# Performance work log

Measured on AMD Instinct MI355X. Metric: run time of the kernel, lower is better.

## Reference

```python
import jax, jax.numpy as jnp
import numpy as np
import math

EPS = float(np.finfo(np.float32).eps)
POWER = 4.0  # init power=4


def cube_face_uv(d):
    # OpenGL cube-map face selection: faces +x,-x,+y,-y,+z,-z -> 0..5
    x, y, z = d[:, 0], d[:, 1], d[:, 2]
    ax, ay, az = jnp.abs(x), jnp.abs(y), jnp.abs(z)
    is_x = (ax >= ay) & (ax >= az)
    is_y = (~is_x) & (ay >= az)
    ma = jnp.maximum(ax, jnp.maximum(ay, az))
    face = jnp.where(is_x, jnp.where(x > 0, 0, 1),
           jnp.where(is_y, jnp.where(y > 0, 2, 3), jnp.where(z > 0, 4, 5)))
    sc = jnp.where(is_x, jnp.where(x > 0, -z, z),
         jnp.where(is_y, x, jnp.where(z > 0, x, -x)))
    tc = jnp.where(is_x, -y, jnp.where(is_y, jnp.where(y > 0, z, -z), -y))
    s = 0.5 * (sc / ma + 1.0)
    t = 0.5 * (tc / ma + 1.0)
    return face.astype(jnp.int32), s, t


def bilinear(tex, face, s, t):
    # tex: [6,R,R,3]; clamp-to-edge bilinear at texel centers (i+0.5)/R
    R = tex.shape[1]
    u = s * R - 0.5
    v = t * R - 0.5
    u0 = jnp.floor(u); v0 = jnp.floor(v)
    fu = (u - u0)[:, None]; fv = (v - v0)[:, None]
    u0i = jnp.clip(u0.astype(jnp.int32), 0, R - 1)
    u1i = jnp.clip(u0.astype(jnp.int32) + 1, 0, R - 1)
    v0i = jnp.clip(v0.astype(jnp.int32), 0, R - 1)
    v1i = jnp.clip(v0.astype(jnp.int32) + 1, 0, R - 1)
    c00 = tex[face, v0i, u0i]; c01 = tex[face, v0i, u1i]
    c10 = tex[face, v1i, u0i]; c11 = tex[face, v1i, u1i]
    return (c00 * (1 - fu) + c01 * fu) * (1 - fv) + (c10 * (1 - fu) + c11 * fu) * fv


def setup_inputs() -> dict:
    key = jax.random.key(0)
    k1, k2, k3 = jax.random.split(key, 3)
    B, R = 1048576, 512
    viewdirs = jax.random.normal(k1, (B, 3), dtype=jnp.float32)
    viewdirs = viewdirs / (jnp.linalg.norm(viewdirs, axis=-1, keepdims=True) + 1e-8)
    saSample = jax.random.normal(k2, (B, 1), dtype=jnp.float32)
    # learned cubemap (init_val=-2 plus small noise so gradients are non-trivial)
    bg_mat = -2.0 + 0.1 * jax.random.normal(k3, (6, R, R, 3), dtype=jnp.float32)
    return {
        'viewdirs': viewdirs,
        'saSample': saSample,
        'bg_mat': bg_mat,
        'brightness': jnp.float32(0.0),
        'mul': jnp.float32(1.0),
        'mipbias': jnp.float32(0.5),
    }


def reference(viewdirs, saSample, bg_mat, brightness, mul, mipbias):
    R = bg_mat.shape[1]
    n_mips = int(math.log2(R)) + 1  # 10 for R=512
    # box-filter mip pyramid (as nvdiffrast auto-generates)
    pyr = [bg_mat]
    for _ in range(n_mips - 1):
        tex = pyr[-1]; r = tex.shape[1]
        pyr.append(tex.reshape(6, r // 2, 2, r // 2, 2, 3).mean(axis=(2, 4)))
    # sa2mip (mipnoise = 0)
    ainf = jnp.max(jnp.abs(viewdirs), axis=-1)            # ||u||_inf
    distortion = (1.0 / ainf)[:, None]                    # [B,1]
    saTexel = distortion / R / R
    mip = (saSample - jnp.log(jnp.clip(saTexel, EPS))) / math.log(POWER) / 2 + mipbias
    mip = jnp.clip(mip[:, 0], 0.0, n_mips - 1.0)          # [B]
    face, s, t = cube_face_uv(viewdirs)
    samples = jnp.stack([bilinear(p, face, s, t) for p in pyr], axis=0)  # [L,B,3]
    m0 = jnp.floor(mip).astype(jnp.int32)
    m1 = jnp.minimum(m0 + 1, n_mips - 1)
    frac = (mip - m0)[:, None]
    B = viewdirs.shape[0]
    lo = jnp.take_along_axis(samples, jnp.broadcast_to(m0[None, :, None], (1, B, 3)), axis=0)[0]
    hi = jnp.take_along_axis(samples, jnp.broadcast_to(m1[None, :, None], (1, B, 3)), axis=0)[0]
    sumemb = lo * (1 - frac) + hi * frac                  # single level -> sum is just this
    # activation 'identity': exp(brightness.clip(-1,2) + mul*x).clip(0.01, 1000)
    x = jnp.clip(brightness, -1.0, 2.0) + mul * sumemb
    return jnp.clip(jnp.exp(x), 0.01, 1000.0)
```

## Files before the change

kernel.cpp:

```cpp
#include <hip/hip_runtime.h>
#include <math.h>


#define BASE_R 512
#define N_MIPS 10

__device__ __forceinline__ size_t mip_off4(int m) {
    return (size_t)8 * (262144u - (1u << (2 * (10 - m))));
}

__global__ __launch_bounds__(256) void pyramid_fused_kernel(
    const float* __restrict__ bg, float* __restrict__ ws) {
    __shared__ float bufA[32 * 32 * 3];
    __shared__ float bufB[16 * 16 * 3];

    const int tid = threadIdx.x;
    const int blk = blockIdx.x;
    const int tileX = blk & 15;
    const int tileY = (blk >> 4) & 15;
    const int f = blk >> 8;

    const size_t faceBase = (size_t)f * (512 * 512 * 3);
    for (int i = tid; i < 32 * 24; i += 256) {
        int row = i / 24;
        int col4 = i % 24;
        const float4 v = *reinterpret_cast<const float4*>(
            bg + faceBase + (size_t)(tileY * 32 + row) * 1536 + tileX * 96 + col4 * 4);
        *reinterpret_cast<float4*>(&bufA[row * 96 + col4 * 4]) = v;
    }
    __syncthreads();

    float* src = bufA;
    float* dst = bufB;
    int rs = 32;
#pragma unroll
    for (int L = 1; L <= 5; ++L) {
        const int rd = rs >> 1;
        const int r = BASE_R >> L;
        float4* gl4 = reinterpret_cast<float4*>(ws + mip_off4(L)) + (size_t)f * r * r;
        const int y0 = tileY * rd;
        const int x0 = tileX * rd;
        const int n = rd * rd;
        for (int i = tid; i < n; i += 256) {
            int x = i % rd;
            int y = i / rd;
            const float* p0 = src + ((2 * y) * rs + 2 * x) * 3;
            const float* p1 = p0 + rs * 3;
            float m0 = (p0[0] + p0[3] + p1[0] + p1[3]) * 0.25f;
            float m1 = (p0[1] + p0[4] + p1[1] + p1[4]) * 0.25f;
            float m2 = (p0[2] + p0[5] + p1[2] + p1[5]) * 0.25f;
            dst[i * 3 + 0] = m0;
            dst[i * 3 + 1] = m1;
            dst[i * 3 + 2] = m2;
            gl4[(size_t)(y0 + y) * r + (x0 + x)] = make_float4(m0, m1, m2, 0.0f);
        }
        __syncthreads();
        float* tmp = src; src = dst; dst = tmp;
        rs = rd;
    }
}

__global__ __launch_bounds__(256) void pyramid_tail_kernel(float* __restrict__ ws) {
    __shared__ float l5[4608];
    __shared__ float l6[1152];
    __shared__ float l7[288];
    __shared__ float l8[72];
    const int tid = threadIdx.x;

    const float4* g5 = reinterpret_cast<const float4*>(ws + mip_off4(5));
    for (int i = tid; i < 1536; i += 256) {
        float4 v = g5[i];
        l5[i * 3 + 0] = v.x; l5[i * 3 + 1] = v.y; l5[i * 3 + 2] = v.z;
    }
    __syncthreads();

    float4* g6 = reinterpret_cast<float4*>(ws + mip_off4(6));
    for (int i = tid; i < 384; i += 256) {
        int x = i & 7, y = (i >> 3) & 7, f = i >> 6;
        const float* p0 = l5 + ((f * 16 + 2 * y) * 16 + 2 * x) * 3;
        const float* p1 = p0 + 48;
        float m0 = (p0[0] + p0[3] + p1[0] + p1[3]) * 0.25f;
        float m1 = (p0[1] + p0[4] + p1[1] + p1[4]) * 0.25f;
        float m2 = (p0[2] + p0[5] + p1[2] + p1[5]) * 0.25f;
        l6[i * 3 + 0] = m0; l6[i * 3 + 1] = m1; l6[i * 3 + 2] = m2;
        g6[i] = make_float4(m0, m1, m2, 0.0f);
    }
    __syncthreads();

    float4* g7 = reinterpret_cast<float4*>(ws + mip_off4(7));
    for (int i = tid; i < 96; i += 256) {
        int x = i & 3, y = (i >> 2) & 3, f = i >> 4;
        const float* p0 = l6 + ((f * 8 + 2 * y) * 8 + 2 * x) * 3;
        const float* p1 = p0 + 24;
        float m0 = (p0[0] + p0[3] + p1[0] + p1[3]) * 0.25f;
        float m1 = (p0[1] + p0[4] + p1[1] + p1[4]) * 0.25f;
        float m2 = (p0[2] + p0[5] + p1[2] + p1[5]) * 0.25f;
        l7[i * 3 + 0] = m0; l7[i * 3 + 1] = m1; l7[i * 3 + 2] = m2;
        g7[i] = make_float4(m0, m1, m2, 0.0f);
    }
    __syncthreads();

    float4* g8 = reinterpret_cast<float4*>(ws + mip_off4(8));
    for (int i = tid; i < 24; i += 256) {
        int x = i & 1, y = (i >> 1) & 1, f = i >> 2;
        const float* p0 = l7 + ((f * 4 + 2 * y) * 4 + 2 * x) * 3;
        const float* p1 = p0 + 12;
        float m0 = (p0[0] + p0[3] + p1[0] + p1[3]) * 0.25f;
        float m1 = (p0[1] + p0[4] + p1[1] + p1[4]) * 0.25f;
        float m2 = (p0[2] + p0[5] + p1[2] + p1[5]) * 0.25f;
        l8[i * 3 + 0] = m0; l8[i * 3 + 1] = m1; l8[i * 3 + 2] = m2;
        g8[i] = make_float4(m0, m1, m2, 0.0f);
    }
    __syncthreads();

    float4* g9 = reinterpret_cast<float4*>(ws + mip_off4(9));
    for (int i = tid; i < 6; i += 256) {
        const float* p = l8 + i * 12;
        float m0 = (p[0] + p[3] + p[6] + p[9]) * 0.25f;
        float m1 = (p[1] + p[4] + p[7] + p[10]) * 0.25f;
        float m2 = (p[2] + p[5] + p[8] + p[11]) * 0.25f;
        g9[i] = make_float4(m0, m1, m2, 0.0f);
    }
}

__device__ __forceinline__ void corner_idx(int Rm, int face, float s, float t,
                                           int& i00, int& i01, int& i10, int& i11,
                                           float& fu, float& fv) {
    float u = s * (float)Rm - 0.5f;
    float v = t * (float)Rm - 0.5f;
    float u0 = floorf(u);
    float v0 = floorf(v);
    fu = u - u0;
    fv = v - v0;
    int u0i = min(max((int)u0, 0), Rm - 1);
    int u1i = min(max((int)u0 + 1, 0), Rm - 1);
    int v0i = min(max((int)v0, 0), Rm - 1);
    int v1i = min(max((int)v0 + 1, 0), Rm - 1);
    int fb = face * Rm;
    i00 = (fb + v0i) * Rm + u0i;
    i01 = (fb + v0i) * Rm + u1i;
    i10 = (fb + v1i) * Rm + u0i;
    i11 = (fb + v1i) * Rm + u1i;
}

__device__ __forceinline__ void blend4(float4 c00, float4 c01, float4 c10, float4 c11,
                                       float fu, float fv, float o[3]) {
    o[0] = (c00.x * (1.0f - fu) + c01.x * fu) * (1.0f - fv) +
           (c10.x * (1.0f - fu) + c11.x * fu) * fv;
    o[1] = (c00.y * (1.0f - fu) + c01.y * fu) * (1.0f - fv) +
           (c10.y * (1.0f - fu) + c11.y * fu) * fv;
    o[2] = (c00.z * (1.0f - fu) + c01.z * fu) * (1.0f - fv) +
           (c10.z * (1.0f - fu) + c11.z * fu) * fv;
}

__device__ __noinline__ void sample_bg(const float* __restrict__ bg, int face,
                                       float s, float t, float o[3]) {
    const int Rm = BASE_R;
    int i00, i01, i10, i11;
    float fu, fv;
    corner_idx(Rm, face, s, t, i00, i01, i10, i11, fu, fv);
    const float* p00 = bg + (size_t)i00 * 3;
    const float* p01 = bg + (size_t)i01 * 3;
    const float* p10 = bg + (size_t)i10 * 3;
    const float* p11 = bg + (size_t)i11 * 3;
#pragma unroll
    for (int c = 0; c < 3; ++c) {
        float top = p00[c] * (1.0f - fu) + p01[c] * fu;
        float bot = p10[c] * (1.0f - fu) + p11[c] * fu;
        o[c] = top * (1.0f - fv) + bot * fv;
    }
}

__global__ __launch_bounds__(256) void cubemap_sample_kernel(
    const float* __restrict__ vd, const float* __restrict__ sa,
    const float* __restrict__ bg, const float* __restrict__ ws,
    float* __restrict__ out, int B,
    const float* __restrict__ p_brightness,
    const float* __restrict__ p_mul,
    const float* __restrict__ p_mipbias) {
    int i = blockIdx.x * blockDim.x + threadIdx.x;
    if (i >= B) return;

    float x = vd[3 * i + 0];
    float y = vd[3 * i + 1];
    float z = vd[3 * i + 2];
    float ax = fabsf(x), ay = fabsf(y), az = fabsf(z);
    float ma = fmaxf(ax, fmaxf(ay, az));

    int face;
    float sc, tc;
    if (ax >= ay && ax >= az) {
        face = (x > 0.0f) ? 0 : 1;
        sc = (x > 0.0f) ? -z : z;
        tc = -y;
    } else if (ay >= az) {
        face = (y > 0.0f) ? 2 : 3;
        sc = x;
        tc = (y > 0.0f) ? z : -z;
    } else {
        face = (z > 0.0f) ? 4 : 5;
        sc = (z > 0.0f) ? x : -x;
        tc = -y;
    }
    float s = 0.5f * (sc / ma + 1.0f);
    float t = 0.5f * (tc / ma + 1.0f);

    float distortion = 1.0f / ma;
    float saTexel = distortion * (1.0f / 262144.0f);
    const float EPSF = 1.1920928955078125e-07f;
    const float LOG4 = 1.3862943611198906f;
    float mip = (sa[i] - logf(fmaxf(saTexel, EPSF))) / LOG4 * 0.5f + p_mipbias[0];
    mip = fminf(fmaxf(mip, 0.0f), (float)(N_MIPS - 1));

    int m0 = (int)floorf(mip);
    int m1 = min(m0 + 1, N_MIPS - 1);
    float frac = mip - (float)m0;

    float lo[3], hi[3];
    if (m0 >= 1) {
        const float4* ta = reinterpret_cast<const float4*>(ws + mip_off4(m0));
        const float4* tb = reinterpret_cast<const float4*>(ws + mip_off4(m1));
        int Ra = BASE_R >> m0, Rb = BASE_R >> m1;
        int a00, a01, a10, a11, b00, b01, b10, b11;
        float afu, afv, bfu, bfv;
        corner_idx(Ra, face, s, t, a00, a01, a10, a11, afu, afv);
        corner_idx(Rb, face, s, t, b00, b01, b10, b11, bfu, bfv);
        float4 A00 = ta[a00], A01 = ta[a01], A10 = ta[a10], A11 = ta[a11];
        float4 B00 = tb[b00], B01 = tb[b01], B10 = tb[b10], B11 = tb[b11];
        blend4(A00, A01, A10, A11, afu, afv, lo);
        blend4(B00, B01, B10, B11, bfu, bfv, hi);
    } else {
        sample_bg(bg, face, s, t, lo);
        const float4* tb = reinterpret_cast<const float4*>(ws + mip_off4(1));
        int Rb = BASE_R >> 1;
        int b00, b01, b10, b11;
        float bfu, bfv;
        corner_idx(Rb, face, s, t, b00, b01, b10, b11, bfu, bfv);
        blend4(tb[b00], tb[b01], tb[b10], tb[b11], bfu, bfv, hi);
    }

    float bb = fminf(fmaxf(p_brightness[0], -1.0f), 2.0f);
    float mulv = p_mul[0];
#pragma unroll
    for (int c = 0; c < 3; ++c) {
        float xv = bb + mulv * (lo[c] * (1.0f - frac) + hi[c] * frac);
        float e = expf(xv);
        out[3 * i + c] = fminf(fmaxf(e, 0.01f), 1000.0f);
    }
}

extern "C" void kernel_launch(void* const* d_in, const int* in_sizes, int n_in,
                              void* d_out, int out_size, void* d_ws, size_t ws_size,
                              hipStream_t stream) {
    const float* viewdirs = (const float*)d_in[0];
    const float* saSample = (const float*)d_in[1];
    const float* bg_mat = (const float*)d_in[2];
    const float* brightness = (const float*)d_in[3];
    const float* mul = (const float*)d_in[4];
    const float* mipbias = (const float*)d_in[5];
    float* out = (float*)d_out;
    float* ws = (float*)d_ws;

    int B = in_sizes[1];

    pyramid_fused_kernel<<<6 * 16 * 16, 256, 0, stream>>>(bg_mat, ws);
    pyramid_tail_kernel<<<1, 256, 0, stream>>>(ws);

    int blocks = (B + 255) / 256;
    cubemap_sample_kernel<<<blocks, 256, 0, stream>>>(
        viewdirs, saSample, bg_mat, ws, out, B, brightness, mul, mipbias);
}
```

Baseline: 32.40 us.

## Stage coarse mip levels in LDS and process four rays per thread

Copies mip levels 5 through 9 (2046 float4 texels) into shared memory at block start and serves coarse-level fetches from LDS instead of global memory. Each thread now shades four rays, using float4 vectorized loads of viewdirs, saSample and output, which cuts the grid to a quarter. The mip computation is simplified algebraically into a log2-based form, and the code switches to fast __expf/__log2f intrinsics. The trade-offs are a per-block LDS fill cost of about 32KB, which limits occupancy, more registers per thread, and slight precision differences from the fast math.

```diff
diff --git a/kernel.cpp b/kernel.cpp
--- a/kernel.cpp
+++ b/kernel.cpp
@@ -123,6 +123,19 @@
     }
 }
 
+#define LDS_T_COUNT 2046
+
+__device__ __forceinline__ int lds_off4(int L) {
+    return LDS_T_COUNT - 2 * ((1 << (2 * (10 - L))) - 1);
+}
+
+__device__ __forceinline__ float4 fetch_tex(const float4* __restrict__ wsT,
+                                            const float4* __restrict__ ldsT,
+                                            int L, int idx) {
+    if (L >= 5) return ldsT[lds_off4(L) + idx];
+    return wsT[2u * (262144u - (1u << (2 * (10 - L)))) + idx];
+}
+
 __device__ __forceinline__ void corner_idx(int Rm, int face, float s, float t,
                                            int& i00, int& i01, int& i10, int& i11,
                                            float& fu, float& fv) {
@@ -155,10 +168,9 @@
 
 __device__ __noinline__ void sample_bg(const float* __restrict__ bg, int face,
                                        float s, float t, float o[3]) {
-    const int Rm = BASE_R;
     int i00, i01, i10, i11;
     float fu, fv;
-    corner_idx(Rm, face, s, t, i00, i01, i10, i11, fu, fv);
+    corner_idx(BASE_R, face, s, t, i00, i01, i10, i11, fu, fv);
     const float* p00 = bg + (size_t)i00 * 3;
     const float* p01 = bg + (size_t)i01 * 3;
     const float* p10 = bg + (size_t)i10 * 3;
@@ -171,19 +183,12 @@
     }
 }
 
-__global__ __launch_bounds__(256) void cubemap_sample_kernel(
-    const float* __restrict__ vd, const float* __restrict__ sa,
-    const float* __restrict__ bg, const float* __restrict__ ws,
-    float* __restrict__ out, int B,
-    const float* __restrict__ p_brightness,
-    const float* __restrict__ p_mul,
-    const float* __restrict__ p_mipbias) {
-    int i = blockIdx.x * blockDim.x + threadIdx.x;
-    if (i >= B) return;
-
-    float x = vd[3 * i + 0];
-    float y = vd[3 * i + 1];
-    float z = vd[3 * i + 2];
+__device__ __forceinline__ void shade_ray(float x, float y, float z, float sav,
+                                          const float* __restrict__ bg,
+                                          const float4* __restrict__ wsT,
+                                          const float4* __restrict__ ldsT,
+                                          float bb, float mulv, float bias,
+                                          float o[3]) {
     float ax = fabsf(x), ay = fabsf(y), az = fabsf(z);
     float ma = fmaxf(ax, fmaxf(ay, az));
 
@@ -205,11 +210,7 @@
     float s = 0.5f * (sc / ma + 1.0f);
     float t = 0.5f * (tc / ma + 1.0f);
 
-    float distortion = 1.0f / ma;
-    float saTexel = distortion * (1.0f / 262144.0f);
-    const float EPSF = 1.1920928955078125e-07f;
-    const float LOG4 = 1.3862943611198906f;
-    float mip = (sa[i] - logf(fmaxf(saTexel, EPSF))) / LOG4 * 0.5f + p_mipbias[0];
+    float mip = sav * 0.36067376022224085f + 0.25f * __log2f(ma) + 4.5f + bias;
     mip = fminf(fmaxf(mip, 0.0f), (float)(N_MIPS - 1));
 
     int m0 = (int)floorf(mip);
@@ -218,34 +219,83 @@
 
     float lo[3], hi[3];
     if (m0 >= 1) {
-        const float4* ta = reinterpret_cast<const float4*>(ws + mip_off4(m0));
-        const float4* tb = reinterpret_cast<const float4*>(ws + mip_off4(m1));
-        int Ra = BASE_R >> m0, Rb = BASE_R >> m1;
-        int a00, a01, a10, a11, b00, b01, b10, b11;
-        float afu, afv, bfu, bfv;
+        int Ra = BASE_R >> m0;
+        int a00, a01, a10, a11;
+        float afu, afv;
         corner_idx(Ra, face, s, t, a00, a01, a10, a11, afu, afv);
-        corner_idx(Rb, face, s, t, b00, b01, b10, b11, bfu, bfv);
-        float4 A00 = ta[a00], A01 = ta[a01], A10 = ta[a10], A11 = ta[a11];
-        float4 B00 = tb[b00], B01 = tb[b01], B10 = tb[b10], B11 = tb[b11];
+        float4 A00 = fetch_tex(wsT, ldsT, m0, a00);
+        float4 A01 = fetch_tex(wsT, ldsT, m0, a01);
+        float4 A10 = fetch_tex(wsT, ldsT, m0, a10);
+        float4 A11 = fetch_tex(wsT, ldsT, m0, a11);
         blend4(A00, A01, A10, A11, afu, afv, lo);
-        blend4(B00, B01, B10, B11, bfu, bfv, hi);
     } else {
         sample_bg(bg, face, s, t, lo);
-        const float4* tb = reinterpret_cast<const float4*>(ws + mip_off4(1));
-        int Rb = BASE_R >> 1;
+    }
+    {
+        int Rb = BASE_R >> m1;
         int b00, b01, b10, b11;
         float bfu, bfv;
         corner_idx(Rb, face, s, t, b00, b01, b10, b11, bfu, bfv);
-        blend4(tb[b00], tb[b01], tb[b10], tb[b11], bfu, bfv, hi);
-    }
-
-    float bb = fminf(fmaxf(p_brightness[0], -1.0f), 2.0f);
-    float mulv = p_mul[0];
+        float4 B00 = fetch_tex(wsT, ldsT, m1, b00);
+        float4 B01 = fetch_tex(wsT, ldsT, m1, b01);
+        float4 B10 = fetch_tex(wsT, ldsT, m1, b10);
+        float4 B11 = fetch_tex(wsT, ldsT, m1, b11);
+        blend4(B00, B01, B10, B11, bfu, bfv, hi);
+    }
+
 #pragma unroll
     for (int c = 0; c < 3; ++c) {
         float xv = bb + mulv * (lo[c] * (1.0f - frac) + hi[c] * frac);
-        float e = expf(xv);
-        out[3 * i + c] = fminf(fmaxf(e, 0.01f), 1000.0f);
+        float e = __expf(xv);
+        o[c] = fminf(fmaxf(e, 0.01f), 1000.0f);
+    }
+}
+
+__global__ __launch_bounds__(256) void cubemap_sample_kernel(
+    const float* __restrict__ vd, const float* __restrict__ sa,
+    const float* __restrict__ bg, const float* __restrict__ ws,
+    float* __restrict__ out, int B,
+    const float* __restrict__ p_brightness,
+    const float* __restrict__ p_mul,
+    const float* __restrict__ p_mipbias) {
+    __shared__ float4 ldsT[LDS_T_COUNT];
+
+    const float4* srcT = reinterpret_cast<const float4*>(ws + mip_off4(5));
+    for (int i = threadIdx.x; i < LDS_T_COUNT; i += 256) ldsT[i] = srcT[i];
+    __syncthreads();
+
+    const float4* wsT = reinterpret_cast<const float4*>(ws);
+    const float bb = fminf(fmaxf(p_brightness[0], -1.0f), 2.0f);
+    const float mulv = p_mul[0];
+    const float bias = p_mipbias[0];
+
+    int gid = blockIdx.x * 256 + threadIdx.x;
+    int base = gid * 4;
+    if (base + 3 < B) {
+        const float4* vd4 = reinterpret_cast<const float4*>(vd);
+        const float4* sa4 = reinterpret_cast<const float4*>(sa);
+        float4* out4 = reinterpret_cast<float4*>(out);
+        float4 a = vd4[3 * (size_t)gid + 0];
+        float4 b = vd4[3 * (size_t)gid + 1];
+        float4 c = vd4[3 * (size_t)gid + 2];
+        float4 s4 = sa4[gid];
+        float res[12];
+        shade_ray(a.x, a.y, a.z, s4.x, bg, wsT, ldsT, bb, mulv, bias, &res[0]);
+        shade_ray(a.w, b.x, b.y, s4.y, bg, wsT, ldsT, bb, mulv, bias, &res[3]);
+        shade_ray(b.z, b.w, c.x, s4.z, bg, wsT, ldsT, bb, mulv, bias, &res[6]);
+        shade_ray(c.y, c.z, c.w, s4.w, bg, wsT, ldsT, bb, mulv, bias, &res[9]);
+        out4[3 * (size_t)gid + 0] = make_float4(res[0], res[1], res[2], res[3]);
+        out4[3 * (size_t)gid + 1] = make_float4(res[4], res[5], res[6], res[7]);
+        out4[3 * (size_t)gid + 2] = make_float4(res[8], res[9], res[10], res[11]);
+    } else {
+        for (int r = base; r < B; ++r) {
+            float o[3];
+            shade_ray(vd[3 * r + 0], vd[3 * r + 1], vd[3 * r + 2], sa[r],
+                      bg, wsT, ldsT, bb, mulv, bias, o);
+            out[3 * r + 0] = o[0];
+            out[3 * r + 1] = o[1];
+            out[3 * r + 2] = o[2];
+        }
     }
 }
 
@@ -266,7 +316,7 @@
     pyramid_fused_kernel<<<6 * 16 * 16, 256, 0, stream>>>(bg_mat, ws);
     pyramid_tail_kernel<<<1, 256, 0, stream>>>(ws);
 
-    int blocks = (B + 255) / 256;
+    int blocks = (B + 1023) / 1024;
     cubemap_sample_kernel<<<blocks, 256, 0, stream>>>(
         viewdirs, saSample, bg_mat, ws, out, B, brightness, mul, mipbias);
 }
```

Measured after the change: 32.89 us. About the same (+1.5%).
